# Performance work log

Hardware: AMD Instinct MI355X
Metric: run time of the kernel (lower is better)

The kernel has to match this reference:

```python
import jax, jax.numpy as jnp
import numpy as np

N_EXC = 1024
N_INH = 256
BATCH = 2048
TAU_E = 10.0
TAU_I = 5.0
DT = 0.1
STEPS = 10


def _ring_weights(sigma, n_exc):
    # Fixed ring topology: Gaussian in wrapped angular distance, row-normalized, zero diagonal.
    angles = jnp.linspace(0.0, 2.0 * jnp.pi, n_exc, dtype=jnp.float32)
    d = angles[None, :] - angles[:, None]                  # [n_exc, n_exc]
    d = jnp.arctan2(jnp.sin(d), jnp.cos(d))                # wrap to (-pi, pi]
    W = jnp.exp(-0.5 * (d / sigma) ** 2)
    W = W / W.sum(axis=1, keepdims=True)
    W = W * (1.0 - jnp.eye(n_exc, dtype=W.dtype))          # fill_diagonal_(0)
    return W


def setup_inputs() -> dict:
    key = jax.random.key(0)
    k_ext, k_h, k_ei, k_ie = jax.random.split(key, 4)
    return {
        "external_input": jax.random.normal(k_ext, (BATCH, N_EXC), dtype=jnp.float32),
        "h": jax.random.uniform(k_h, (BATCH, N_EXC), dtype=jnp.float32),
        "sigma_ee": jnp.float32(0.5),
        "W_EI": jax.random.normal(k_ei, (N_EXC, N_INH), dtype=jnp.float32) * 0.1,
        "W_IE": jax.random.normal(k_ie, (N_INH, N_EXC), dtype=jnp.float32) * 0.1,
        "g_ee": jnp.float32(1.0),
        "g_ei": jnp.float32(1.5),
        "g_ie": jnp.float32(2.0),
        "g_input": jnp.float32(1.0),
        "noise_rate_e": jnp.float32(0.1),
        "noise_rate_i": jnp.float32(0.05),
        "steps": STEPS,
    }


def reference(external_input, h, sigma_ee, W_EI, W_IE, g_ee, g_ei, g_ie, g_input,
              noise_rate_e, noise_rate_i, steps):
    B, n_exc = external_input.shape
    n_inh = W_EI.shape[1]
    # sigma_ee is constant across steps -> compute the ring weights once (same math).
    W_EE = _ring_weights(sigma_ee, n_exc)
    r_e0 = h                                               # eval path with h provided
    r_i0 = jnp.zeros((B, n_inh), dtype=h.dtype)
    noise_key = jax.random.key(42)

    def step(carry, t):
        r_e, r_i = carry
        ke, ki = jax.random.split(jax.random.fold_in(noise_key, t))
        # batched versions of the per-sample matmuls
        input_e = (g_ee * jnp.einsum('ij,bj->bi', W_EE, r_e)
                   - g_ie * jnp.einsum('bj,ji->bi', r_i, W_IE)
                   + g_input * external_input)
        input_i = g_ei * jnp.einsum('be,ei->bi', r_e, W_EI)
        # Poisson noise, mean-subtracted (torch.poisson is non-differentiable).
        pe = jax.lax.stop_gradient(
            jax.random.poisson(ke, jax.lax.stop_gradient(noise_rate_e), input_e.shape)
        ).astype(input_e.dtype)
        pi = jax.lax.stop_gradient(
            jax.random.poisson(ki, jax.lax.stop_gradient(noise_rate_i), input_i.shape)
        ).astype(input_i.dtype)
        input_e = input_e + (pe - noise_rate_e)
        input_i = input_i + (pi - noise_rate_i)
        r_e = jax.nn.relu(r_e + DT * (-r_e + jax.nn.relu(input_e)) / TAU_E)
        r_i = jax.nn.relu(r_i + DT * (-r_i + jax.nn.relu(input_i)) / TAU_I)
        return (r_e, r_i), None

    (r_e, r_i), _ = jax.lax.scan(step, (r_e0, r_i0), jnp.arange(steps))
    return r_e
```

## Files before the change

kernel.cpp:

```cpp
#include <hip/hip_runtime.h>
#include <cstdint>


#define N_EXC 1024
#define N_INH 256
#define BATCH 2048
#define STEPS 10
#define MAX_POIS 32

typedef short s16x8 __attribute__((ext_vector_type(8)));
typedef float f32x4 __attribute__((ext_vector_type(4)));

typedef __attribute__((address_space(1))) const void GV;
typedef __attribute__((address_space(3))) void LV;

struct U2 { uint32_t x, y; };

__device__ __forceinline__ uint32_t rotl32(uint32_t v, int r) {
  return (v << r) | (v >> (32 - r));
}

__device__ __forceinline__ U2 threefry(U2 k, uint32_t x0, uint32_t x1) {
  uint32_t ks0 = k.x, ks1 = k.y, ks2 = k.x ^ k.y ^ 0x1BD11BDAu;
  x0 += ks0; x1 += ks1;
#define TF_R4(a,b,c,d) \
  x0 += x1; x1 = rotl32(x1,a); x1 ^= x0; \
  x0 += x1; x1 = rotl32(x1,b); x1 ^= x0; \
  x0 += x1; x1 = rotl32(x1,c); x1 ^= x0; \
  x0 += x1; x1 = rotl32(x1,d); x1 ^= x0;
  TF_R4(13,15,26,6)  x0 += ks1; x1 += ks2 + 1u;
  TF_R4(17,29,16,24) x0 += ks2; x1 += ks0 + 2u;
  TF_R4(13,15,26,6)  x0 += ks0; x1 += ks1 + 3u;
  TF_R4(17,29,16,24) x0 += ks1; x1 += ks2 + 4u;
  TF_R4(13,15,26,6)  x0 += ks2; x1 += ks0 + 5u;
#undef TF_R4
  U2 r; r.x = x0; r.y = x1; return r;
}

__device__ __forceinline__ float poisson_mean_sub(uint32_t e,
                                                  const U2* __restrict__ sk,
                                                  float lam) {
  float neg_lam = -lam;
  float lp = 0.0f;
  int k = 0;
#pragma unroll 1
  for (int n = 0; n < MAX_POIS; ++n) {
    if (!(lp > neg_lam)) break;
    k++;
    U2 h = threefry(sk[n], 0u, e);
    uint32_t bits = h.x ^ h.y;
    float u = __uint_as_float((bits >> 9) | 0x3f800000u) - 1.0f;
    lp += logf(u);
  }
  return (float)(k - 1) - lam;
}

__device__ __forceinline__ unsigned short f2b(float f) {
  uint32_t u = __float_as_uint(f);
  return (unsigned short)((u + 0x7FFFu + ((u >> 16) & 1u)) >> 16);
}

__device__ __forceinline__ void gload16(const void* g, void* l) {
  __builtin_amdgcn_global_load_lds((GV*)g, (LV*)l, 16, 0, 0);
}

__global__ void keys_kernel(U2* subk_e, U2* subk_i) {
  int tid = threadIdx.x;
  if (tid >= 2 * STEPS) return;
  int t = tid >> 1;
  bool is_i = tid & 1;
  U2 base; base.x = 0u; base.y = 42u;
  U2 folded = threefry(base, 0u, (uint32_t)t);
  U2 ke = threefry(folded, 0u, 0u);
  U2 ki = threefry(folded, 0u, 1u);
  U2 rng = is_i ? ki : ke;
  U2* dst = (is_i ? subk_i : subk_e) + t * MAX_POIS;
  for (int n = 0; n < MAX_POIS; ++n) {
    dst[n] = threefry(rng, 0u, 1u);
    rng = threefry(rng, 0u, 0u);
  }
}

__global__ __launch_bounds__(256) void wee_kernel(const float* __restrict__ sigma_p,
                                                  unsigned short* __restrict__ W) {
  int i = blockIdx.x;
  int tid = threadIdx.x;
  float sigma = *sigma_p;
  const float twopi = 6.28318530717958647692f;
  const float delta = twopi / 1023.0f;
  float ai = (float)i * delta;
  float w[4];
  float s = 0.0f;
#pragma unroll
  for (int q = 0; q < 4; ++q) {
    int j = tid + q * 256;
    float aj = (float)j * delta;
    float d = aj - ai;
    float wd = atan2f(sinf(d), cosf(d));
    float x = wd / sigma;
    float v = expf(-0.5f * x * x);
    w[q] = v;
    s += v;
  }
  __shared__ float red[256];
  red[tid] = s;
  __syncthreads();
  for (int off = 128; off > 0; off >>= 1) {
    if (tid < off) red[tid] += red[tid + off];
    __syncthreads();
  }
  float sum = red[0];
#pragma unroll
  for (int q = 0; q < 4; ++q) {
    int j = tid + q * 256;
    W[i * N_EXC + j] = (j == i) ? (unsigned short)0 : f2b(w[q] / sum);
  }
}

__global__ void setup_kernel(const float* __restrict__ W_EI, const float* __restrict__ W_IE,
                             const float* __restrict__ h,
                             unsigned short* __restrict__ W_EIT,
                             unsigned short* __restrict__ W_IET,
                             unsigned short* __restrict__ hb) {
  int tid = blockIdx.x * blockDim.x + threadIdx.x;
  int nt = gridDim.x * blockDim.x;
  for (int i = tid; i < BATCH * N_EXC; i += nt) hb[i] = f2b(h[i]);
  for (int i = tid; i < N_INH * N_EXC; i += nt) {
    int r = i >> 10, c = i & 1023;
    W_EIT[i] = f2b(W_EI[c * N_INH + r]);
  }
  for (int i = tid; i < N_EXC * N_INH; i += nt) {
    int r = i >> 8, c = i & 255;
    W_IET[i] = f2b(W_IE[c * N_EXC + r]);
  }
}

#define PIPE_GEMM(APTR, LDA, AROW0, BPTR, LDB, BROW0, KLEN, ACC)                \
  {                                                                             \
    const int NT = (KLEN) / 64;                                                 \
    int c0 = wave * 128 + lane;                                                 \
    int c1 = c0 + 64;                                                           \
    int r0 = c0 >> 3, q0 = ((c0 & 7) ^ (r0 & 7)) << 3;                          \
    int r1 = c1 >> 3, q1 = ((c1 & 7) ^ (r1 & 7)) << 3;                          \
    const unsigned short* ap0 = (APTR) + (size_t)((AROW0) + r0) * (LDA) + q0;   \
    const unsigned short* ap1 = (APTR) + (size_t)((AROW0) + r1) * (LDA) + q1;   \
    const unsigned short* bp0 = (BPTR) + (size_t)((BROW0) + r0) * (LDB) + q0;   \
    const unsigned short* bp1 = (BPTR) + (size_t)((BROW0) + r1) * (LDB) + q1;   \
    char* la0 = (char*)As + wave * 2048;                                        \
    char* la1 = la0 + 1024;                                                     \
    char* lb0 = (char*)Bs + wave * 2048;                                        \
    char* lb1 = lb0 + 1024;                                                     \
    gload16(ap0, la0); gload16(ap1, la1);                                       \
    gload16(bp0, lb0); gload16(bp1, lb1);                                       \
    int cur = 0;                                                                \
    int raf0 = wr * 32 + l16, raf1 = raf0 + 16;                                 \
    int rbf0 = wc * 32 + l16, rbf1 = rbf0 + 16;                                 \
    int aA0 = (raf0 << 7) | ((lhi ^ (raf0 & 7)) << 4);                          \
    int aA1 = (raf1 << 7) | ((lhi ^ (raf1 & 7)) << 4);                          \
    int aB0 = (rbf0 << 7) | ((lhi ^ (rbf0 & 7)) << 4);                          \
    int aB1 = (rbf1 << 7) | ((lhi ^ (rbf1 & 7)) << 4);                          \
    for (int kt = 0; kt < NT; ++kt) {                                           \
      __syncthreads();                                                          \
      if (kt + 1 < NT) {                                                        \
        int k0 = (kt + 1) * 64;                                                 \
        int nb = (cur ^ 1) * 8192;                                              \
        gload16(ap0 + k0, la0 + nb); gload16(ap1 + k0, la1 + nb);               \
        gload16(bp0 + k0, lb0 + nb); gload16(bp1 + k0, lb1 + nb);               \
      }                                                                         \
      const char* ab = (const char*)As + cur * 8192;                            \
      const char* bb = (const char*)Bs + cur * 8192;                            \
      _Pragma("unroll")                                                         \
      for (int ks = 0; ks < 2; ++ks) {                                          \
        int kx = ks << 6;                                                       \
        s16x8 af0 = *(const s16x8*)(ab + (aA0 ^ kx));                           \
        s16x8 af1 = *(const s16x8*)(ab + (aA1 ^ kx));                           \
        s16x8 bf0 = *(const s16x8*)(bb + (aB0 ^ kx));                           \
        s16x8 bf1 = *(const s16x8*)(bb + (aB1 ^ kx));                           \
        ACC[0][0] = __builtin_amdgcn_mfma_f32_16x16x32_bf16(af0, bf0, ACC[0][0], 0, 0, 0); \
        ACC[0][1] = __builtin_amdgcn_mfma_f32_16x16x32_bf16(af0, bf1, ACC[0][1], 0, 0, 0); \
        ACC[1][0] = __builtin_amdgcn_mfma_f32_16x16x32_bf16(af1, bf0, ACC[1][0], 0, 0, 0); \
        ACC[1][1] = __builtin_amdgcn_mfma_f32_16x16x32_bf16(af1, bf1, ACC[1][1], 0, 0, 0); \
      }                                                                         \
      cur ^= 1;                                                                 \
    }                                                                           \
  }

__global__ __launch_bounds__(256) void step_kernel(
    const float* __restrict__ re_in, const unsigned short* __restrict__ reb_in,
    const float* __restrict__ ri_in, const unsigned short* __restrict__ rib_in,
    const unsigned short* __restrict__ W_EEb, const unsigned short* __restrict__ W_IET,
    const unsigned short* __restrict__ W_EIT,
    const float* __restrict__ ext,
    const float* __restrict__ sc_gee, const float* __restrict__ sc_gei,
    const float* __restrict__ sc_gie, const float* __restrict__ sc_gin,
    const float* __restrict__ sc_rate_e, const float* __restrict__ sc_rate_i,
    const U2* __restrict__ subk_e, const U2* __restrict__ subk_i,
    float* __restrict__ re_out, unsigned short* __restrict__ reb_out,
    float* __restrict__ ri_out, unsigned short* __restrict__ rib_out) {
  __shared__ __align__(16) short As[2 * 4096];
  __shared__ __align__(16) short Bs[2 * 4096];
  int tid = threadIdx.x;
  int lane = tid & 63;
  int wave = tid >> 6;
  int wr = wave >> 1, wc = wave & 1;
  int l16 = lane & 15, lhi = lane >> 4;
  int b0 = blockIdx.x * 64;
  bool is_e = blockIdx.y < 16;
  int i0 = (is_e ? blockIdx.y : (blockIdx.y - 16)) * 64;

  f32x4 acc[2][2] = {};
  f32x4 acc2[2][2] = {};

  if (is_e) {
    PIPE_GEMM(reb_in, N_EXC, b0, W_EEb, N_EXC, i0, N_EXC, acc);
    if (rib_in != nullptr) {
      PIPE_GEMM(rib_in, N_INH, b0, W_IET, N_INH, i0, N_INH, acc2);
    }
    float gee = *sc_gee, gie = *sc_gie, gin = *sc_gin, rate = *sc_rate_e;
#pragma unroll
    for (int mm = 0; mm < 2; ++mm)
#pragma unroll
      for (int nn = 0; nn < 2; ++nn)
#pragma unroll
        for (int q = 0; q < 4; ++q) {
          int row = b0 + wr * 32 + mm * 16 + lhi * 4 + q;
          int col = i0 + wc * 32 + nn * 16 + l16;
          int idx = row * N_EXC + col;
          float val = gee * acc[mm][nn][q] - gie * acc2[mm][nn][q] + gin * ext[idx];
          val += poisson_mean_sub((uint32_t)idx, subk_e, rate);
          float ro = re_in[idx];
          float rn = ro + (0.1f * (fmaxf(val, 0.0f) - ro)) / 10.0f;
          rn = fmaxf(rn, 0.0f);
          re_out[idx] = rn;
          reb_out[idx] = f2b(rn);
        }
  } else {
    PIPE_GEMM(reb_in, N_EXC, b0, W_EIT, N_EXC, i0, N_EXC, acc);
    float gei = *sc_gei, rate = *sc_rate_i;
#pragma unroll
    for (int mm = 0; mm < 2; ++mm)
#pragma unroll
      for (int nn = 0; nn < 2; ++nn)
#pragma unroll
        for (int q = 0; q < 4; ++q) {
          int row = b0 + wr * 32 + mm * 16 + lhi * 4 + q;
          int col = i0 + wc * 32 + nn * 16 + l16;
          int idx = row * N_INH + col;
          float val = gei * acc[mm][nn][q];
          val += poisson_mean_sub((uint32_t)idx, subk_i, rate);
          float rio = (ri_in != nullptr) ? ri_in[idx] : 0.0f;
          float rn = rio + (0.1f * (fmaxf(val, 0.0f) - rio)) / 5.0f;
          rn = fmaxf(rn, 0.0f);
          ri_out[idx] = rn;
          rib_out[idx] = f2b(rn);
        }
  }
}

extern "C" void kernel_launch(void* const* d_in, const int* in_sizes, int n_in,
                              void* d_out, int out_size, void* d_ws, size_t ws_size,
                              hipStream_t stream) {
  const float* ext    = (const float*)d_in[0];
  const float* h      = (const float*)d_in[1];
  const float* sigma  = (const float*)d_in[2];
  const float* W_EI   = (const float*)d_in[3];
  const float* W_IE   = (const float*)d_in[4];
  const float* g_ee   = (const float*)d_in[5];
  const float* g_ei   = (const float*)d_in[6];
  const float* g_ie   = (const float*)d_in[7];
  const float* g_in   = (const float*)d_in[8];
  const float* rate_e = (const float*)d_in[9];
  const float* rate_i = (const float*)d_in[10];

  char* ws = (char*)d_ws;
  unsigned short* W_EEb = (unsigned short*)ws; ws += (size_t)N_EXC * N_EXC * 2;
  unsigned short* W_EIT = (unsigned short*)ws; ws += (size_t)N_INH * N_EXC * 2;
  unsigned short* W_IET = (unsigned short*)ws; ws += (size_t)N_EXC * N_INH * 2;
  float* reA            = (float*)ws;          ws += (size_t)BATCH * N_EXC * 4;
  unsigned short* rebA  = (unsigned short*)ws; ws += (size_t)BATCH * N_EXC * 2;
  unsigned short* rebB  = (unsigned short*)ws; ws += (size_t)BATCH * N_EXC * 2;
  float* riA            = (float*)ws;          ws += (size_t)BATCH * N_INH * 4;
  float* riB            = (float*)ws;          ws += (size_t)BATCH * N_INH * 4;
  unsigned short* ribA  = (unsigned short*)ws; ws += (size_t)BATCH * N_INH * 2;
  unsigned short* ribB  = (unsigned short*)ws; ws += (size_t)BATCH * N_INH * 2;
  U2* subk_e            = (U2*)ws;             ws += (size_t)STEPS * MAX_POIS * sizeof(U2);
  U2* subk_i            = (U2*)ws;             ws += (size_t)STEPS * MAX_POIS * sizeof(U2);
  float* re_dout = (float*)d_out;

  wee_kernel<<<dim3(N_EXC), dim3(256), 0, stream>>>(sigma, W_EEb);
  setup_kernel<<<dim3(512), dim3(256), 0, stream>>>(W_EI, W_IE, h, W_EIT, W_IET, rebB);
  keys_kernel<<<dim3(1), dim3(64), 0, stream>>>(subk_e, subk_i);

  for (int t = 0; t < STEPS; ++t) {
    const float* re_in          = (t == 0) ? h : ((t & 1) ? reA : re_dout);
    float* re_out               = (t & 1) ? re_dout : reA;
    const unsigned short* rb_in = (t & 1) ? rebA : rebB;
    unsigned short* rb_out      = (t & 1) ? rebB : rebA;
    const float* ri_in          = (t == 0) ? nullptr : ((t & 1) ? riA : riB);
    float* ri_out               = (t & 1) ? riB : riA;
    const unsigned short* ib_in = (t == 0) ? nullptr : ((t & 1) ? ribA : ribB);
    unsigned short* ib_out      = (t & 1) ? ribB : ribA;

    step_kernel<<<dim3(BATCH / 64, 20), dim3(256), 0, stream>>>(
        re_in, rb_in, ri_in, ib_in, W_EEb, W_IET, W_EIT, ext,
        g_ee, g_ei, g_ie, g_in, rate_e, rate_i,
        subk_e + t * MAX_POIS, subk_i + t * MAX_POIS,
        re_out, rb_out, ri_out, ib_out);
  }
}
```

Measured before the change: 394.0 us.

## Precompute next-step Poisson noise in extra blocks and triple-buffer GEMM loads

Poisson noise generation moves out of the GEMM epilogue. Extra blocks in each step launch compute the next step's noise counts into uint8 buffers, which the current step's GEMM blocks then read, and a separate kernel seeds step 0. This is meant to overlap the RNG work with the matrix multiplies instead of serialising it after them. The GEMM pipeline also goes from double to triple buffering in LDS, using explicit vmcnt waits, to hide more load latency. The cost is extra LDS per block, more workspace memory traffic, and an added barrier between the two E GEMMs.

```diff
diff --git a/kernel.cpp b/kernel.cpp
--- a/kernel.cpp
+++ b/kernel.cpp
@@ -7,6 +7,9 @@
 #define BATCH 2048
 #define STEPS 10
 #define MAX_POIS 32
+#define NE_TOT (BATCH * N_EXC)
+#define NTOT   (NE_TOT + BATCH * N_INH)
+#define NZ_SLICES 8
 
 typedef short s16x8 __attribute__((ext_vector_type(8)));
 typedef float f32x4 __attribute__((ext_vector_type(4)));
@@ -37,24 +40,6 @@
   U2 r; r.x = x0; r.y = x1; return r;
 }
 
-__device__ __forceinline__ float poisson_mean_sub(uint32_t e,
-                                                  const U2* __restrict__ sk,
-                                                  float lam) {
-  float neg_lam = -lam;
-  float lp = 0.0f;
-  int k = 0;
-#pragma unroll 1
-  for (int n = 0; n < MAX_POIS; ++n) {
-    if (!(lp > neg_lam)) break;
-    k++;
-    U2 h = threefry(sk[n], 0u, e);
-    uint32_t bits = h.x ^ h.y;
-    float u = __uint_as_float((bits >> 9) | 0x3f800000u) - 1.0f;
-    lp += logf(u);
-  }
-  return (float)(k - 1) - lam;
-}
-
 __device__ __forceinline__ unsigned short f2b(float f) {
   uint32_t u = __float_as_uint(f);
   return (unsigned short)((u + 0x7FFFu + ((u >> 16) & 1u)) >> 16);
@@ -62,6 +47,30 @@
 
 __device__ __forceinline__ void gload16(const void* g, void* l) {
   __builtin_amdgcn_global_load_lds((GV*)g, (LV*)l, 16, 0, 0);
+}
+
+__device__ void gen_noise(int f0, int stride,
+                          const U2* __restrict__ ske, const U2* __restrict__ ski,
+                          float lam_e, float lam_i,
+                          uint8_t* __restrict__ nze, uint8_t* __restrict__ nzi) {
+  for (int f = f0; f < NTOT; f += stride) {
+    bool ii = f >= NE_TOT;
+    uint32_t e = ii ? (uint32_t)(f - NE_TOT) : (uint32_t)f;
+    const U2* sk = ii ? ski : ske;
+    float neg = ii ? -lam_i : -lam_e;
+    float lp = 0.0f;
+    int k = 0;
+#pragma unroll 1
+    for (int n = 0; n < MAX_POIS; ++n) {
+      if (!(lp > neg)) break;
+      k++;
+      U2 h = threefry(sk[n], 0u, e);
+      uint32_t bits = h.x ^ h.y;
+      float u = __uint_as_float((bits >> 9) | 0x3f800000u) - 1.0f;
+      lp += logf(u);
+    }
+    (ii ? nzi : nze)[e] = (uint8_t)(k - 1);
+  }
 }
 
 __global__ void keys_kernel(U2* subk_e, U2* subk_i) {
@@ -79,6 +88,14 @@
     dst[n] = threefry(rng, 0u, 1u);
     rng = threefry(rng, 0u, 0u);
   }
+}
+
+__global__ __launch_bounds__(256) void noise0_kernel(
+    const U2* __restrict__ subk_e, const U2* __restrict__ subk_i,
+    const float* __restrict__ sc_rate_e, const float* __restrict__ sc_rate_i,
+    uint8_t* __restrict__ nze, uint8_t* __restrict__ nzi) {
+  int flat = blockIdx.x * 256 + threadIdx.x;
+  gen_noise(flat, gridDim.x * 256, subk_e, subk_i, *sc_rate_e, *sc_rate_i, nze, nzi);
 }
 
 __global__ __launch_bounds__(256) void wee_kernel(const float* __restrict__ sigma_p,
@@ -152,7 +169,9 @@
     char* lb1 = lb0 + 1024;                                                     \
     gload16(ap0, la0); gload16(ap1, la1);                                       \
     gload16(bp0, lb0); gload16(bp1, lb1);                                       \
-    int cur = 0;                                                                \
+    gload16(ap0 + 64, la0 + 8192); gload16(ap1 + 64, la1 + 8192);               \
+    gload16(bp0 + 64, lb0 + 8192); gload16(bp1 + 64, lb1 + 8192);               \
+    int rd = 0, wr2 = 16384;                                                    \
     int raf0 = wr * 32 + l16, raf1 = raf0 + 16;                                 \
     int rbf0 = wc * 32 + l16, rbf1 = rbf0 + 16;                                 \
     int aA0 = (raf0 << 7) | ((lhi ^ (raf0 & 7)) << 4);                          \
@@ -160,15 +179,18 @@
     int aB0 = (rbf0 << 7) | ((lhi ^ (rbf0 & 7)) << 4);                          \
     int aB1 = (rbf1 << 7) | ((lhi ^ (rbf1 & 7)) << 4);                          \
     for (int kt = 0; kt < NT; ++kt) {                                           \
-      __syncthreads();                                                          \
-      if (kt + 1 < NT) {                                                        \
-        int k0 = (kt + 1) * 64;                                                 \
-        int nb = (cur ^ 1) * 8192;                                              \
-        gload16(ap0 + k0, la0 + nb); gload16(ap1 + k0, la1 + nb);               \
-        gload16(bp0 + k0, lb0 + nb); gload16(bp1 + k0, lb1 + nb);               \
+      if (kt < NT - 1) {                                                        \
+        asm volatile("s_waitcnt vmcnt(4)\n\ts_barrier" ::: "memory");           \
+      } else {                                                                  \
+        asm volatile("s_waitcnt vmcnt(0)\n\ts_barrier" ::: "memory");           \
       }                                                                         \
-      const char* ab = (const char*)As + cur * 8192;                            \
-      const char* bb = (const char*)Bs + cur * 8192;                            \
+      if (kt + 2 < NT) {                                                        \
+        int k0 = (kt + 2) * 64;                                                 \
+        gload16(ap0 + k0, la0 + wr2); gload16(ap1 + k0, la1 + wr2);             \
+        gload16(bp0 + k0, lb0 + wr2); gload16(bp1 + k0, lb1 + wr2);             \
+      }                                                                         \
+      const char* ab = (const char*)As + rd;                                    \
+      const char* bb = (const char*)Bs + rd;                                    \
       _Pragma("unroll")                                                         \
       for (int ks = 0; ks < 2; ++ks) {                                          \
         int kx = ks << 6;                                                       \
@@ -181,7 +203,8 @@
         ACC[1][0] = __builtin_amdgcn_mfma_f32_16x16x32_bf16(af1, bf0, ACC[1][0], 0, 0, 0); \
         ACC[1][1] = __builtin_amdgcn_mfma_f32_16x16x32_bf16(af1, bf1, ACC[1][1], 0, 0, 0); \
       }                                                                         \
-      cur ^= 1;                                                                 \
+      rd = (rd == 16384) ? 0 : rd + 8192;                                       \
+      wr2 = (wr2 == 16384) ? 0 : wr2 + 8192;                                    \
     }                                                                           \
   }
 
@@ -194,12 +217,24 @@
     const float* __restrict__ sc_gee, const float* __restrict__ sc_gei,
     const float* __restrict__ sc_gie, const float* __restrict__ sc_gin,
     const float* __restrict__ sc_rate_e, const float* __restrict__ sc_rate_i,
-    const U2* __restrict__ subk_e, const U2* __restrict__ subk_i,
+    const uint8_t* __restrict__ nz_e_in, const uint8_t* __restrict__ nz_i_in,
+    uint8_t* __restrict__ nz_e_out, uint8_t* __restrict__ nz_i_out,
+    const U2* __restrict__ subk_e_next, const U2* __restrict__ subk_i_next,
     float* __restrict__ re_out, unsigned short* __restrict__ reb_out,
     float* __restrict__ ri_out, unsigned short* __restrict__ rib_out) {
-  __shared__ __align__(16) short As[2 * 4096];
-  __shared__ __align__(16) short Bs[2 * 4096];
+  __shared__ __align__(16) short As[3 * 4096];
+  __shared__ __align__(16) short Bs[3 * 4096];
   int tid = threadIdx.x;
+
+  if (blockIdx.y >= 20) {
+    if (nz_e_out != nullptr) {
+      int flat = ((blockIdx.y - 20) * gridDim.x + blockIdx.x) * 256 + tid;
+      gen_noise(flat, NZ_SLICES * 32 * 256, subk_e_next, subk_i_next,
+                *sc_rate_e, *sc_rate_i, nz_e_out, nz_i_out);
+    }
+    return;
+  }
+
   int lane = tid & 63;
   int wave = tid >> 6;
   int wr = wave >> 1, wc = wave & 1;
@@ -214,6 +249,7 @@
   if (is_e) {
     PIPE_GEMM(reb_in, N_EXC, b0, W_EEb, N_EXC, i0, N_EXC, acc);
     if (rib_in != nullptr) {
+      __syncthreads();
       PIPE_GEMM(rib_in, N_INH, b0, W_IET, N_INH, i0, N_INH, acc2);
     }
     float gee = *sc_gee, gie = *sc_gie, gin = *sc_gin, rate = *sc_rate_e;
@@ -227,7 +263,7 @@
           int col = i0 + wc * 32 + nn * 16 + l16;
           int idx = row * N_EXC + col;
           float val = gee * acc[mm][nn][q] - gie * acc2[mm][nn][q] + gin * ext[idx];
-          val += poisson_mean_sub((uint32_t)idx, subk_e, rate);
+          val += (float)nz_e_in[idx] - rate;
           float ro = re_in[idx];
           float rn = ro + (0.1f * (fmaxf(val, 0.0f) - ro)) / 10.0f;
           rn = fmaxf(rn, 0.0f);
@@ -247,7 +283,7 @@
           int col = i0 + wc * 32 + nn * 16 + l16;
           int idx = row * N_INH + col;
           float val = gei * acc[mm][nn][q];
-          val += poisson_mean_sub((uint32_t)idx, subk_i, rate);
+          val += (float)nz_i_in[idx] - rate;
           float rio = (ri_in != nullptr) ? ri_in[idx] : 0.0f;
           float rn = rio + (0.1f * (fmaxf(val, 0.0f) - rio)) / 5.0f;
           rn = fmaxf(rn, 0.0f);
@@ -283,6 +319,10 @@
   float* riB            = (float*)ws;          ws += (size_t)BATCH * N_INH * 4;
   unsigned short* ribA  = (unsigned short*)ws; ws += (size_t)BATCH * N_INH * 2;
   unsigned short* ribB  = (unsigned short*)ws; ws += (size_t)BATCH * N_INH * 2;
+  uint8_t* nzE0         = (uint8_t*)ws;        ws += (size_t)NE_TOT;
+  uint8_t* nzE1         = (uint8_t*)ws;        ws += (size_t)NE_TOT;
+  uint8_t* nzI0         = (uint8_t*)ws;        ws += (size_t)BATCH * N_INH;
+  uint8_t* nzI1         = (uint8_t*)ws;        ws += (size_t)BATCH * N_INH;
   U2* subk_e            = (U2*)ws;             ws += (size_t)STEPS * MAX_POIS * sizeof(U2);
   U2* subk_i            = (U2*)ws;             ws += (size_t)STEPS * MAX_POIS * sizeof(U2);
   float* re_dout = (float*)d_out;
@@ -290,6 +330,8 @@
   wee_kernel<<<dim3(N_EXC), dim3(256), 0, stream>>>(sigma, W_EEb);
   setup_kernel<<<dim3(512), dim3(256), 0, stream>>>(W_EI, W_IE, h, W_EIT, W_IET, rebB);
   keys_kernel<<<dim3(1), dim3(64), 0, stream>>>(subk_e, subk_i);
+  noise0_kernel<<<dim3(512), dim3(256), 0, stream>>>(subk_e, subk_i, rate_e, rate_i,
+                                                     nzE0, nzI0);
 
   for (int t = 0; t < STEPS; ++t) {
     const float* re_in          = (t == 0) ? h : ((t & 1) ? reA : re_dout);
@@ -300,11 +342,16 @@
     float* ri_out               = (t & 1) ? riB : riA;
     const unsigned short* ib_in = (t == 0) ? nullptr : ((t & 1) ? ribA : ribB);
     unsigned short* ib_out      = (t & 1) ? ribB : ribA;
-
-    step_kernel<<<dim3(BATCH / 64, 20), dim3(256), 0, stream>>>(
+    const uint8_t* nze_in       = (t & 1) ? nzE1 : nzE0;
+    const uint8_t* nzi_in       = (t & 1) ? nzI1 : nzI0;
+    uint8_t* nze_out            = (t + 1 < STEPS) ? ((t & 1) ? nzE0 : nzE1) : nullptr;
+    uint8_t* nzi_out            = (t + 1 < STEPS) ? ((t & 1) ? nzI0 : nzI1) : nullptr;
+
+    step_kernel<<<dim3(BATCH / 64, 20 + NZ_SLICES), dim3(256), 0, stream>>>(
         re_in, rb_in, ri_in, ib_in, W_EEb, W_IET, W_EIT, ext,
         g_ee, g_ei, g_ie, g_in, rate_e, rate_i,
-        subk_e + t * MAX_POIS, subk_i + t * MAX_POIS,
+        nze_in, nzi_in, nze_out, nzi_out,
+        subk_e + (t + 1) * MAX_POIS, subk_i + (t + 1) * MAX_POIS,
         re_out, rb_out, ri_out, ib_out);
   }
 }
```

New measurement: 670.0 us. 1.7x slower.

## Fuse all time steps into one persistent kernel with grid barriers

Applied to the files above, without the earlier changes.

Replaces the ten per-step kernel launches with a single persistent kernel of 640 blocks that loops over steps and synchronizes through atomic-counter grid barriers in workspace memory. This targets per-launch overhead and the idle tail between dependent launches. It depends on all blocks being co-resident, checked via an occupancy query with a fallback to the old launch loop, and adds spin-wait barrier latency plus fences every step.

```diff
diff --git a/kernel.cpp b/kernel.cpp
--- a/kernel.cpp
+++ b/kernel.cpp
@@ -7,6 +7,9 @@
 #define BATCH 2048
 #define STEPS 10
 #define MAX_POIS 32
+#define GRID_X 32
+#define GRID_Y 20
+#define NBLK (GRID_X * GRID_Y)
 
 typedef short s16x8 __attribute__((ext_vector_type(8)));
 typedef float f32x4 __attribute__((ext_vector_type(4)));
@@ -62,6 +65,19 @@
 
 __device__ __forceinline__ void gload16(const void* g, void* l) {
   __builtin_amdgcn_global_load_lds((GV*)g, (LV*)l, 16, 0, 0);
+}
+
+__device__ __forceinline__ void grid_barrier(int* ctr) {
+  __syncthreads();
+  if (threadIdx.x == 0) {
+    __threadfence();
+    __hip_atomic_fetch_add(ctr, 1, __ATOMIC_ACQ_REL, __HIP_MEMORY_SCOPE_AGENT);
+    while (__hip_atomic_load(ctr, __ATOMIC_ACQUIRE, __HIP_MEMORY_SCOPE_AGENT) < NBLK) {
+      __builtin_amdgcn_s_sleep(8);
+    }
+  }
+  __syncthreads();
+  __threadfence();
 }
 
 __global__ void keys_kernel(U2* subk_e, U2* subk_i) {
@@ -185,6 +201,57 @@
     }                                                                           \
   }
 
+#define STEP_BODY(RE_IN, RB_IN, RI_IN, IB_IN, W_EE_, W_IET_, W_EIT_, EXT_,      \
+                  GEE, GEI, GIE, GIN, RATE_E, RATE_I, SKE, SKI,                 \
+                  RE_OUT, RB_OUT, RI_OUT, IB_OUT)                               \
+  {                                                                             \
+    f32x4 acc[2][2] = {};                                                       \
+    f32x4 acc2[2][2] = {};                                                      \
+    if (is_e) {                                                                 \
+      PIPE_GEMM(RB_IN, N_EXC, b0, W_EE_, N_EXC, i0, N_EXC, acc);                \
+      if ((IB_IN) != nullptr) {                                                 \
+        PIPE_GEMM(IB_IN, N_INH, b0, W_IET_, N_INH, i0, N_INH, acc2);            \
+      }                                                                         \
+      _Pragma("unroll")                                                         \
+      for (int mm = 0; mm < 2; ++mm)                                            \
+        _Pragma("unroll")                                                       \
+        for (int nn = 0; nn < 2; ++nn)                                          \
+          _Pragma("unroll")                                                     \
+          for (int q = 0; q < 4; ++q) {                                         \
+            int row = b0 + wr * 32 + mm * 16 + lhi * 4 + q;                     \
+            int col = i0 + wc * 32 + nn * 16 + l16;                             \
+            int idx = row * N_EXC + col;                                        \
+            float val = (GEE) * acc[mm][nn][q] - (GIE) * acc2[mm][nn][q]        \
+                      + (GIN) * (EXT_)[idx];                                    \
+            val += poisson_mean_sub((uint32_t)idx, SKE, RATE_E);                \
+            float ro = (RE_IN)[idx];                                            \
+            float rn = ro + (0.1f * (fmaxf(val, 0.0f) - ro)) / 10.0f;           \
+            rn = fmaxf(rn, 0.0f);                                               \
+            (RE_OUT)[idx] = rn;                                                 \
+            (RB_OUT)[idx] = f2b(rn);                                            \
+          }                                                                     \
+    } else {                                                                    \
+      PIPE_GEMM(RB_IN, N_EXC, b0, W_EIT_, N_EXC, i0, N_EXC, acc);               \
+      _Pragma("unroll")                                                         \
+      for (int mm = 0; mm < 2; ++mm)                                            \
+        _Pragma("unroll")                                                       \
+        for (int nn = 0; nn < 2; ++nn)                                          \
+          _Pragma("unroll")                                                     \
+          for (int q = 0; q < 4; ++q) {                                         \
+            int row = b0 + wr * 32 + mm * 16 + lhi * 4 + q;                     \
+            int col = i0 + wc * 32 + nn * 16 + l16;                             \
+            int idx = row * N_INH + col;                                        \
+            float val = (GEI) * acc[mm][nn][q];                                 \
+            val += poisson_mean_sub((uint32_t)idx, SKI, RATE_I);                \
+            float rio = ((RI_IN) != nullptr) ? (RI_IN)[idx] : 0.0f;             \
+            float rn = rio + (0.1f * (fmaxf(val, 0.0f) - rio)) / 5.0f;          \
+            rn = fmaxf(rn, 0.0f);                                               \
+            (RI_OUT)[idx] = rn;                                                 \
+            (IB_OUT)[idx] = f2b(rn);                                            \
+          }                                                                     \
+    }                                                                           \
+  }
+
 __global__ __launch_bounds__(256) void step_kernel(
     const float* __restrict__ re_in, const unsigned short* __restrict__ reb_in,
     const float* __restrict__ ri_in, const unsigned short* __restrict__ rib_in,
@@ -207,53 +274,58 @@
   int b0 = blockIdx.x * 64;
   bool is_e = blockIdx.y < 16;
   int i0 = (is_e ? blockIdx.y : (blockIdx.y - 16)) * 64;
-
-  f32x4 acc[2][2] = {};
-  f32x4 acc2[2][2] = {};
-
-  if (is_e) {
-    PIPE_GEMM(reb_in, N_EXC, b0, W_EEb, N_EXC, i0, N_EXC, acc);
-    if (rib_in != nullptr) {
-      PIPE_GEMM(rib_in, N_INH, b0, W_IET, N_INH, i0, N_INH, acc2);
-    }
-    float gee = *sc_gee, gie = *sc_gie, gin = *sc_gin, rate = *sc_rate_e;
-#pragma unroll
-    for (int mm = 0; mm < 2; ++mm)
-#pragma unroll
-      for (int nn = 0; nn < 2; ++nn)
-#pragma unroll
-        for (int q = 0; q < 4; ++q) {
-          int row = b0 + wr * 32 + mm * 16 + lhi * 4 + q;
-          int col = i0 + wc * 32 + nn * 16 + l16;
-          int idx = row * N_EXC + col;
-          float val = gee * acc[mm][nn][q] - gie * acc2[mm][nn][q] + gin * ext[idx];
-          val += poisson_mean_sub((uint32_t)idx, subk_e, rate);
-          float ro = re_in[idx];
-          float rn = ro + (0.1f * (fmaxf(val, 0.0f) - ro)) / 10.0f;
-          rn = fmaxf(rn, 0.0f);
-          re_out[idx] = rn;
-          reb_out[idx] = f2b(rn);
-        }
-  } else {
-    PIPE_GEMM(reb_in, N_EXC, b0, W_EIT, N_EXC, i0, N_EXC, acc);
-    float gei = *sc_gei, rate = *sc_rate_i;
-#pragma unroll
-    for (int mm = 0; mm < 2; ++mm)
-#pragma unroll
-      for (int nn = 0; nn < 2; ++nn)
-#pragma unroll
-        for (int q = 0; q < 4; ++q) {
-          int row = b0 + wr * 32 + mm * 16 + lhi * 4 + q;
-          int col = i0 + wc * 32 + nn * 16 + l16;
-          int idx = row * N_INH + col;
-          float val = gei * acc[mm][nn][q];
-          val += poisson_mean_sub((uint32_t)idx, subk_i, rate);
-          float rio = (ri_in != nullptr) ? ri_in[idx] : 0.0f;
-          float rn = rio + (0.1f * (fmaxf(val, 0.0f) - rio)) / 5.0f;
-          rn = fmaxf(rn, 0.0f);
-          ri_out[idx] = rn;
-          rib_out[idx] = f2b(rn);
-        }
+  float gee = *sc_gee, gei = *sc_gei, gie = *sc_gie, gin = *sc_gin;
+  float rate_e = *sc_rate_e, rate_i = *sc_rate_i;
+  STEP_BODY(re_in, reb_in, ri_in, rib_in, W_EEb, W_IET, W_EIT, ext,
+            gee, gei, gie, gin, rate_e, rate_i, subk_e, subk_i,
+            re_out, reb_out, ri_out, rib_out)
+}
+
+struct SP {
+  const float* ext; const float* h;
+  const unsigned short* W_EEb; const unsigned short* W_IET; const unsigned short* W_EIT;
+  const float *gee, *gei, *gie, *gin, *rate_e, *rate_i;
+  const U2 *subk_e, *subk_i;
+  float *reA, *reD;
+  unsigned short *rebA, *rebB;
+  float *riA, *riB;
+  unsigned short *ribA, *ribB;
+  int* bar;
+};
+
+__global__ __launch_bounds__(256, 3) void fused_kernel(SP p) {
+  __shared__ __align__(16) short As[2 * 4096];
+  __shared__ __align__(16) short Bs[2 * 4096];
+  int tid = threadIdx.x;
+  int lane = tid & 63;
+  int wave = tid >> 6;
+  int wr = wave >> 1, wc = wave & 1;
+  int l16 = lane & 15, lhi = lane >> 4;
+  int b0 = blockIdx.x * 64;
+  bool is_e = blockIdx.y < 16;
+  int i0 = (is_e ? blockIdx.y : (blockIdx.y - 16)) * 64;
+
+  float gee = *p.gee, gei = *p.gei, gie = *p.gie, gin = *p.gin;
+  float rate_e = *p.rate_e, rate_i = *p.rate_i;
+
+#pragma unroll 1
+  for (int t = 0; t < STEPS; ++t) {
+    const float* re_in          = (t == 0) ? p.h : ((t & 1) ? p.reA : p.reD);
+    float* re_out               = (t & 1) ? p.reD : p.reA;
+    const unsigned short* rb_in = (t & 1) ? p.rebA : p.rebB;
+    unsigned short* rb_out      = (t & 1) ? p.rebB : p.rebA;
+    const float* ri_in          = (t == 0) ? nullptr : ((t & 1) ? p.riA : p.riB);
+    float* ri_out               = (t & 1) ? p.riB : p.riA;
+    const unsigned short* ib_in = (t == 0) ? nullptr : ((t & 1) ? p.ribA : p.ribB);
+    unsigned short* ib_out      = (t & 1) ? p.ribB : p.ribA;
+    const U2* ske = p.subk_e + t * MAX_POIS;
+    const U2* ski = p.subk_i + t * MAX_POIS;
+
+    STEP_BODY(re_in, rb_in, ri_in, ib_in, p.W_EEb, p.W_IET, p.W_EIT, p.ext,
+              gee, gei, gie, gin, rate_e, rate_i, ske, ski,
+              re_out, rb_out, ri_out, ib_out)
+
+    if (t + 1 < STEPS) grid_barrier(p.bar + t);
   }
 }
 
@@ -285,26 +357,48 @@
   unsigned short* ribB  = (unsigned short*)ws; ws += (size_t)BATCH * N_INH * 2;
   U2* subk_e            = (U2*)ws;             ws += (size_t)STEPS * MAX_POIS * sizeof(U2);
   U2* subk_i            = (U2*)ws;             ws += (size_t)STEPS * MAX_POIS * sizeof(U2);
+  int* bar              = (int*)ws;            ws += (size_t)STEPS * sizeof(int);
   float* re_dout = (float*)d_out;
 
+  hipMemsetAsync(bar, 0, STEPS * sizeof(int), stream);
   wee_kernel<<<dim3(N_EXC), dim3(256), 0, stream>>>(sigma, W_EEb);
   setup_kernel<<<dim3(512), dim3(256), 0, stream>>>(W_EI, W_IE, h, W_EIT, W_IET, rebB);
   keys_kernel<<<dim3(1), dim3(64), 0, stream>>>(subk_e, subk_i);
 
-  for (int t = 0; t < STEPS; ++t) {
-    const float* re_in          = (t == 0) ? h : ((t & 1) ? reA : re_dout);
-    float* re_out               = (t & 1) ? re_dout : reA;
-    const unsigned short* rb_in = (t & 1) ? rebA : rebB;
-    unsigned short* rb_out      = (t & 1) ? rebB : rebA;
-    const float* ri_in          = (t == 0) ? nullptr : ((t & 1) ? riA : riB);
-    float* ri_out               = (t & 1) ? riB : riA;
-    const unsigned short* ib_in = (t == 0) ? nullptr : ((t & 1) ? ribA : ribB);
-    unsigned short* ib_out      = (t & 1) ? ribB : ribA;
-
-    step_kernel<<<dim3(BATCH / 64, 20), dim3(256), 0, stream>>>(
-        re_in, rb_in, ri_in, ib_in, W_EEb, W_IET, W_EIT, ext,
-        g_ee, g_ei, g_ie, g_in, rate_e, rate_i,
-        subk_e + t * MAX_POIS, subk_i + t * MAX_POIS,
-        re_out, rb_out, ri_out, ib_out);
-  }
-}
+  int nb = 0;
+  hipError_t oe = hipOccupancyMaxActiveBlocksPerMultiprocessor(
+      &nb, (const void*)fused_kernel, 256, 0);
+  bool use_fused = (oe == hipSuccess) && (nb >= 3);
+
+  if (use_fused) {
+    SP p;
+    p.ext = ext; p.h = h;
+    p.W_EEb = W_EEb; p.W_IET = W_IET; p.W_EIT = W_EIT;
+    p.gee = g_ee; p.gei = g_ei; p.gie = g_ie; p.gin = g_in;
+    p.rate_e = rate_e; p.rate_i = rate_i;
+    p.subk_e = subk_e; p.subk_i = subk_i;
+    p.reA = reA; p.reD = re_dout;
+    p.rebA = rebA; p.rebB = rebB;
+    p.riA = riA; p.riB = riB;
+    p.ribA = ribA; p.ribB = ribB;
+    p.bar = bar;
+    fused_kernel<<<dim3(GRID_X, GRID_Y), dim3(256), 0, stream>>>(p);
+  } else {
+    for (int t = 0; t < STEPS; ++t) {
+      const float* re_in          = (t == 0) ? h : ((t & 1) ? reA : re_dout);
+      float* re_out               = (t & 1) ? re_dout : reA;
+      const unsigned short* rb_in = (t & 1) ? rebA : rebB;
+      unsigned short* rb_out      = (t & 1) ? rebB : rebA;
+      const float* ri_in          = (t == 0) ? nullptr : ((t & 1) ? riA : riB);
+      float* ri_out               = (t & 1) ? riB : riA;
+      const unsigned short* ib_in = (t == 0) ? nullptr : ((t & 1) ? ribA : ribB);
+      unsigned short* ib_out      = (t & 1) ? ribB : ribA;
+
+      step_kernel<<<dim3(GRID_X, GRID_Y), dim3(256), 0, stream>>>(
+          re_in, rb_in, ri_in, ib_in, W_EEb, W_IET, W_EIT, ext,
+          g_ee, g_ei, g_ie, g_in, rate_e, rate_i,
+          subk_e + t * MAX_POIS, subk_i + t * MAX_POIS,
+          re_out, rb_out, ri_out, ib_out);
+    }
+  }
+}
```

Result: no change. 401.2 us (+1.8%).

## Split-K the step GEMM into two partials and move epilogue to separate kernel

Applied to the files above, without the earlier changes.

The per-step fused GEMM+epilogue kernel is split into a split-K GEMM kernel (grid z=2, each half of K) writing fp32 partial sums, and a vectorized elementwise epilogue kernel that sums partials, adds input and Poisson noise, and updates state. The intent is to double the number of GEMM blocks (640 to 1280) to fill more CUs, and to move the costly RNG epilogue into a fully parallel vectorized pass. In exchange it adds an extra kernel launch per step and extra global traffic writing and reading fp32 partial buffers.

```diff
diff --git a/kernel.cpp b/kernel.cpp
--- a/kernel.cpp
+++ b/kernel.cpp
@@ -7,9 +7,12 @@
 #define BATCH 2048
 #define STEPS 10
 #define MAX_POIS 32
+#define NE_TOT (BATCH * N_EXC)
+#define NTOT   (NE_TOT + BATCH * N_INH)
 
 typedef short s16x8 __attribute__((ext_vector_type(8)));
 typedef float f32x4 __attribute__((ext_vector_type(4)));
+typedef unsigned short u16x4 __attribute__((ext_vector_type(4)));
 
 typedef __attribute__((address_space(1))) const void GV;
 typedef __attribute__((address_space(3))) void LV;
@@ -185,18 +188,14 @@
     }                                                                           \
   }
 
-__global__ __launch_bounds__(256) void step_kernel(
-    const float* __restrict__ re_in, const unsigned short* __restrict__ reb_in,
-    const float* __restrict__ ri_in, const unsigned short* __restrict__ rib_in,
+__global__ __launch_bounds__(256) void gemm_partial(
+    const unsigned short* __restrict__ reb_in, const unsigned short* __restrict__ rib_in,
     const unsigned short* __restrict__ W_EEb, const unsigned short* __restrict__ W_IET,
     const unsigned short* __restrict__ W_EIT,
-    const float* __restrict__ ext,
-    const float* __restrict__ sc_gee, const float* __restrict__ sc_gei,
-    const float* __restrict__ sc_gie, const float* __restrict__ sc_gin,
-    const float* __restrict__ sc_rate_e, const float* __restrict__ sc_rate_i,
-    const U2* __restrict__ subk_e, const U2* __restrict__ subk_i,
-    float* __restrict__ re_out, unsigned short* __restrict__ reb_out,
-    float* __restrict__ ri_out, unsigned short* __restrict__ rib_out) {
+    const float* __restrict__ sc_gee, const float* __restrict__ sc_gie,
+    const float* __restrict__ sc_gei,
+    float* __restrict__ pe0, float* __restrict__ pe1,
+    float* __restrict__ pi0, float* __restrict__ pi1) {
   __shared__ __align__(16) short As[2 * 4096];
   __shared__ __align__(16) short Bs[2 * 4096];
   int tid = threadIdx.x;
@@ -207,16 +206,20 @@
   int b0 = blockIdx.x * 64;
   bool is_e = blockIdx.y < 16;
   int i0 = (is_e ? blockIdx.y : (blockIdx.y - 16)) * 64;
+  int z = blockIdx.z;
 
   f32x4 acc[2][2] = {};
   f32x4 acc2[2][2] = {};
 
   if (is_e) {
-    PIPE_GEMM(reb_in, N_EXC, b0, W_EEb, N_EXC, i0, N_EXC, acc);
+    int zoff = z * 512;
+    PIPE_GEMM(reb_in + zoff, N_EXC, b0, W_EEb + zoff, N_EXC, i0, 512, acc);
     if (rib_in != nullptr) {
-      PIPE_GEMM(rib_in, N_INH, b0, W_IET, N_INH, i0, N_INH, acc2);
+      int zoff2 = z * 128;
+      PIPE_GEMM(rib_in + zoff2, N_INH, b0, W_IET + zoff2, N_INH, i0, 128, acc2);
     }
-    float gee = *sc_gee, gie = *sc_gie, gin = *sc_gin, rate = *sc_rate_e;
+    float gee = *sc_gee, gie = *sc_gie;
+    float* pz = z ? pe1 : pe0;
 #pragma unroll
     for (int mm = 0; mm < 2; ++mm)
 #pragma unroll
@@ -225,18 +228,13 @@
         for (int q = 0; q < 4; ++q) {
           int row = b0 + wr * 32 + mm * 16 + lhi * 4 + q;
           int col = i0 + wc * 32 + nn * 16 + l16;
-          int idx = row * N_EXC + col;
-          float val = gee * acc[mm][nn][q] - gie * acc2[mm][nn][q] + gin * ext[idx];
-          val += poisson_mean_sub((uint32_t)idx, subk_e, rate);
-          float ro = re_in[idx];
-          float rn = ro + (0.1f * (fmaxf(val, 0.0f) - ro)) / 10.0f;
-          rn = fmaxf(rn, 0.0f);
-          re_out[idx] = rn;
-          reb_out[idx] = f2b(rn);
+          pz[row * N_EXC + col] = gee * acc[mm][nn][q] - gie * acc2[mm][nn][q];
         }
   } else {
-    PIPE_GEMM(reb_in, N_EXC, b0, W_EIT, N_EXC, i0, N_EXC, acc);
-    float gei = *sc_gei, rate = *sc_rate_i;
+    int zoff = z * 512;
+    PIPE_GEMM(reb_in + zoff, N_EXC, b0, W_EIT + zoff, N_EXC, i0, 512, acc);
+    float gei = *sc_gei;
+    float* pz = z ? pi1 : pi0;
 #pragma unroll
     for (int mm = 0; mm < 2; ++mm)
 #pragma unroll
@@ -245,15 +243,61 @@
         for (int q = 0; q < 4; ++q) {
           int row = b0 + wr * 32 + mm * 16 + lhi * 4 + q;
           int col = i0 + wc * 32 + nn * 16 + l16;
-          int idx = row * N_INH + col;
-          float val = gei * acc[mm][nn][q];
-          val += poisson_mean_sub((uint32_t)idx, subk_i, rate);
-          float rio = (ri_in != nullptr) ? ri_in[idx] : 0.0f;
-          float rn = rio + (0.1f * (fmaxf(val, 0.0f) - rio)) / 5.0f;
-          rn = fmaxf(rn, 0.0f);
-          ri_out[idx] = rn;
-          rib_out[idx] = f2b(rn);
+          pz[row * N_INH + col] = gei * acc[mm][nn][q];
         }
+  }
+}
+
+__global__ __launch_bounds__(256) void epi_kernel(
+    const float* __restrict__ pe0, const float* __restrict__ pe1,
+    const float* __restrict__ pi0, const float* __restrict__ pi1,
+    const float* __restrict__ ext,
+    const float* __restrict__ re_in, const float* __restrict__ ri_in,
+    const float* __restrict__ sc_gin,
+    const float* __restrict__ sc_rate_e, const float* __restrict__ sc_rate_i,
+    const U2* __restrict__ subk_e, const U2* __restrict__ subk_i,
+    float* __restrict__ re_out, unsigned short* __restrict__ reb_out,
+    float* __restrict__ ri_out, unsigned short* __restrict__ rib_out) {
+  int gtid = blockIdx.x * 256 + threadIdx.x;
+  int base = gtid * 4;
+  if (base < NE_TOT) {
+    float gin = *sc_gin, rate = *sc_rate_e;
+    f32x4 a0 = *(const f32x4*)&pe0[base];
+    f32x4 a1 = *(const f32x4*)&pe1[base];
+    f32x4 ex = *(const f32x4*)&ext[base];
+    f32x4 ro = *(const f32x4*)&re_in[base];
+    f32x4 rn;
+    u16x4 rb;
+#pragma unroll
+    for (int j = 0; j < 4; ++j) {
+      float val = a0[j] + a1[j] + gin * ex[j];
+      val += poisson_mean_sub((uint32_t)(base + j), subk_e, rate);
+      float r = ro[j] + (0.1f * (fmaxf(val, 0.0f) - ro[j])) / 10.0f;
+      r = fmaxf(r, 0.0f);
+      rn[j] = r;
+      rb[j] = f2b(r);
+    }
+    *(f32x4*)&re_out[base] = rn;
+    *(u16x4*)&reb_out[base] = rb;
+  } else {
+    int e0 = base - NE_TOT;
+    float rate = *sc_rate_i;
+    f32x4 a0 = *(const f32x4*)&pi0[e0];
+    f32x4 a1 = *(const f32x4*)&pi1[e0];
+    f32x4 rn;
+    u16x4 rb;
+#pragma unroll
+    for (int j = 0; j < 4; ++j) {
+      float val = a0[j] + a1[j];
+      val += poisson_mean_sub((uint32_t)(e0 + j), subk_i, rate);
+      float rio = (ri_in != nullptr) ? ri_in[e0 + j] : 0.0f;
+      float r = rio + (0.1f * (fmaxf(val, 0.0f) - rio)) / 5.0f;
+      r = fmaxf(r, 0.0f);
+      rn[j] = r;
+      rb[j] = f2b(r);
+    }
+    *(f32x4*)&ri_out[e0] = rn;
+    *(u16x4*)&rib_out[e0] = rb;
   }
 }
 
@@ -283,6 +327,10 @@
   float* riB            = (float*)ws;          ws += (size_t)BATCH * N_INH * 4;
   unsigned short* ribA  = (unsigned short*)ws; ws += (size_t)BATCH * N_INH * 2;
   unsigned short* ribB  = (unsigned short*)ws; ws += (size_t)BATCH * N_INH * 2;
+  float* pe0            = (float*)ws;          ws += (size_t)BATCH * N_EXC * 4;
+  float* pe1            = (float*)ws;          ws += (size_t)BATCH * N_EXC * 4;
+  float* pi0            = (float*)ws;          ws += (size_t)BATCH * N_INH * 4;
+  float* pi1            = (float*)ws;          ws += (size_t)BATCH * N_INH * 4;
   U2* subk_e            = (U2*)ws;             ws += (size_t)STEPS * MAX_POIS * sizeof(U2);
   U2* subk_i            = (U2*)ws;             ws += (size_t)STEPS * MAX_POIS * sizeof(U2);
   float* re_dout = (float*)d_out;
@@ -301,9 +349,11 @@
     const unsigned short* ib_in = (t == 0) ? nullptr : ((t & 1) ? ribA : ribB);
     unsigned short* ib_out      = (t & 1) ? ribB : ribA;
 
-    step_kernel<<<dim3(BATCH / 64, 20), dim3(256), 0, stream>>>(
-        re_in, rb_in, ri_in, ib_in, W_EEb, W_IET, W_EIT, ext,
-        g_ee, g_ei, g_ie, g_in, rate_e, rate_i,
+    gemm_partial<<<dim3(BATCH / 64, 20, 2), dim3(256), 0, stream>>>(
+        rb_in, ib_in, W_EEb, W_IET, W_EIT, g_ee, g_ie, g_ei, pe0, pe1, pi0, pi1);
+
+    epi_kernel<<<dim3(NTOT / 4 / 256), dim3(256), 0, stream>>>(
+        pe0, pe1, pi0, pi1, ext, re_in, ri_in, g_in, rate_e, rate_i,
         subk_e + t * MAX_POIS, subk_i + t * MAX_POIS,
         re_out, rb_out, ri_out, ib_out);
   }
```

Measured after the change: 397.8 us. Within noise of the previous version (+1.0%).
